# Kernel tuning notes

Hardware: AMD Instinct MI355X
Metric: run time of the kernel (lower is better)

The kernel has to match this reference:

```python
import jax, jax.numpy as jnp
import numpy as np

N, D_IN, D_OUT = 8192, 1024, 1024

def setup_inputs() -> dict:
    key = jax.random.key(0)
    kx, kq, kk, kv = jax.random.split(key, 4)
    # Linear weights stored as [in_dim, out_dim] (torch stores [out,in]; we pre-transpose)
    s = 1.0 / np.sqrt(D_IN)
    return {
        "x": jax.random.normal(kx, (N, D_IN), dtype=jnp.float32),
        "Wq": jax.random.uniform(kq, (D_IN, D_OUT), dtype=jnp.float32, minval=-s, maxval=s),
        "Wk": jax.random.uniform(kk, (D_IN, D_OUT), dtype=jnp.float32, minval=-s, maxval=s),
        "Wv": jax.random.uniform(kv, (D_IN, D_OUT), dtype=jnp.float32, minval=-s, maxval=s),
    }

def reference(x, Wq, Wk, Wv):
    # Faithful to source: query_w = keys_L(x), key_w = queries_L(x) -- a name swap
    # that is just a relabeling of independent random weights. The earlier
    # parameter matmuls in the source are dead code (overwritten) and omitted.
    q = x @ Wk          # [N, D_OUT]
    k = x @ Wq          # [N, D_OUT]
    v = x @ Wv          # [N, D_OUT]
    scores = (q @ k.T) / jnp.sqrt(jnp.asarray(D_OUT, dtype=q.dtype))  # [N, N]
    weights = jax.nn.softmax(scores, axis=-1)
    return weights @ v  # [N, D_OUT]
```

## Files before the change

kernel.cpp:

```cpp
#include <hip/hip_runtime.h>
#include <hip/hip_bf16.h>
#include <stdint.h>

typedef __bf16 v8bf __attribute__((ext_vector_type(8)));
typedef __bf16 v4bf __attribute__((ext_vector_type(4)));
typedef float  v4f  __attribute__((ext_vector_type(4)));

#define AS1 __attribute__((address_space(1)))
#define AS3 __attribute__((address_space(3)))

__device__ __forceinline__ void load16_lds(const void* g, void* l) {
  __builtin_amdgcn_global_load_lds((const AS1 uint32_t*)g, (AS3 uint32_t*)l, 16, 0, 0);
}

__global__ __launch_bounds__(256) void k_cvt_x(const float* __restrict__ x,
                                               __bf16* __restrict__ xb) {
  size_t i = ((size_t)blockIdx.x * 256 + threadIdx.x) * 4;
  float4 f = *(const float4*)(x + i);
  v4bf b; b[0] = (__bf16)f.x; b[1] = (__bf16)f.y; b[2] = (__bf16)f.z; b[3] = (__bf16)f.w;
  *(v4bf*)(xb + i) = b;
}

__global__ __launch_bounds__(256) void k_wtrans(const float* __restrict__ W,
                                                __bf16* __restrict__ Wt) {
  __shared__ float tile[64][65];
  int r0 = blockIdx.x * 64, c0 = blockIdx.y * 64;
  int t = threadIdx.x;
  #pragma unroll
  for (int p = 0; p < 16; p++) {
    int idx = p * 256 + t; int rr = idx >> 6, cc = idx & 63;
    tile[rr][cc] = W[(size_t)(r0 + rr) * 1024 + c0 + cc];
  }
  __syncthreads();
  #pragma unroll
  for (int p = 0; p < 16; p++) {
    int idx = p * 256 + t; int rr = idx >> 6, cc = idx & 63;
    Wt[(size_t)(c0 + rr) * 1024 + r0 + cc] = (__bf16)tile[cc][rr];
  }
}

__global__ __launch_bounds__(256) void k_vtrans(const __bf16* __restrict__ V,
                                                __bf16* __restrict__ Vt) {
  __shared__ __bf16 tile[64][66];
  int r0 = blockIdx.x * 64, c0 = blockIdx.y * 64;
  int t = threadIdx.x;
  #pragma unroll
  for (int p = 0; p < 16; p++) {
    int idx = p * 256 + t; int rr = idx >> 6, cc = idx & 63;
    tile[rr][cc] = V[(size_t)(r0 + rr) * 1024 + c0 + cc];
  }
  __syncthreads();
  #pragma unroll
  for (int p = 0; p < 16; p++) {
    int idx = p * 256 + t; int rr = idx >> 6, cc = idx & 63;
    Vt[(size_t)(c0 + rr) * 8192 + r0 + cc] = tile[cc][rr];
  }
}

__global__ __launch_bounds__(256) void k_zero(float* __restrict__ p) {
  size_t i = ((size_t)blockIdx.x * 256 + threadIdx.x) * 4;
  *(float4*)(p + i) = make_float4(0.f, 0.f, 0.f, 0.f);
}

__global__ __launch_bounds__(256) void k_combine(const float* __restrict__ p0,
                                                 const float* __restrict__ p1,
                                                 const float* __restrict__ rowsum,
                                                 float* __restrict__ out) {
  size_t i = ((size_t)blockIdx.x * 256 + threadIdx.x) * 4;
  float4 a = *(const float4*)(p0 + i);
  float4 b = *(const float4*)(p1 + i);
  float ri = 1.0f / rowsum[i >> 10];
  float4 o;
  o.x = (a.x + b.x) * ri; o.y = (a.y + b.y) * ri;
  o.z = (a.z + b.z) * ri; o.w = (a.w + b.w) * ri;
  *(float4*)(out + i) = o;
}

template <int EPI>
__global__ __launch_bounds__(512, 2) void gemm256(
    const __bf16* __restrict__ A, const __bf16* __restrict__ B,
    void* __restrict__ Cout, int M, int N, int KS, int lda, int ldb,
    __bf16* __restrict__ qp, __bf16* __restrict__ kp, __bf16* __restrict__ vp,
    float* __restrict__ rowsum)
{
  __shared__ __bf16 Asm[2][256 * 64];
  __shared__ __bf16 Bsm[2][256 * 64];

  const int tid  = threadIdx.x;
  const int wave = tid >> 6, lane = tid & 63;
  const int wm = (wave >> 2) * 128;
  const int wn = (wave & 3) * 64;
  const size_t m0 = (size_t)blockIdx.x * 256;
  const size_t n0 = (size_t)blockIdx.y * 256;
  const int NT = KS >> 6;
  const int kz = blockIdx.z * KS;

  const int srow8   = lane >> 3;
  const int sgchunk = (lane & 7) ^ srow8;
  const int fr  = lane & 15;
  const int hi  = lane >> 4;
  const int flo = lane & 7;

  const size_t slda = (size_t)lda, sldb = (size_t)ldb;

  v4f acc[8][4];
  #pragma unroll
  for (int i = 0; i < 8; i++)
    #pragma unroll
    for (int j = 0; j < 4; j++) acc[i][j] = (v4f)0.f;

  auto stageA = [&](int v, int R0) {
    const int kk = kz + (v < NT ? v : NT - 1) * 64;
    const __bf16* s = A + (m0 + R0 + wave * 8 + srow8) * slda + kk + sgchunk * 8;
    __bf16* d = &Asm[v & 1][(R0 + wave * 8) * 64];
    load16_lds(s, d);
    load16_lds(s + 64 * slda, d + 64 * 64);
  };
  auto stageB = [&](int v, int R0) {
    const int kk = kz + (v < NT ? v : NT - 1) * 64;
    const __bf16* s = B + (n0 + R0 + wave * 8 + srow8) * sldb + kk + sgchunk * 8;
    __bf16* d = &Bsm[v & 1][(R0 + wave * 8) * 64];
    load16_lds(s, d);
    load16_lds(s + 64 * sldb, d + 64 * 64);
  };

  stageA(0, 0); stageA(0, 128);
  stageB(0, 0); stageB(0, 128);
  stageB(1, 0); stageB(1, 128);
  asm volatile("s_waitcnt vmcnt(4)" ::: "memory");
  __builtin_amdgcn_s_barrier();

  v8bf aq[4][2], bA[2][2], bB[2][2];

  for (int t = 0; t < NT; t++) {
    const int c = t & 1;
    const __bf16* Ab = Asm[c];
    const __bf16* Bb = Bsm[c];

    #pragma unroll
    for (int i = 0; i < 4; i++)
      #pragma unroll
      for (int h = 0; h < 2; h++)
        aq[i][h] = *(const v8bf*)(Ab + (wm + i * 16 + fr) * 64 + ((((h << 2) | hi) ^ flo) * 8));
    #pragma unroll
    for (int j = 0; j < 2; j++)
      #pragma unroll
      for (int h = 0; h < 2; h++)
        bA[j][h] = *(const v8bf*)(Bb + (wn + j * 16 + fr) * 64 + ((((h << 2) | hi) ^ flo) * 8));
    stageA(t + 1, 0);
    __builtin_amdgcn_s_barrier();
    asm volatile("s_waitcnt lgkmcnt(0)" ::: "memory");
    __builtin_amdgcn_sched_barrier(0);
    __builtin_amdgcn_s_setprio(1);
    #pragma unroll
    for (int h = 0; h < 2; h++)
      #pragma unroll
      for (int i = 0; i < 4; i++)
        #pragma unroll
        for (int j = 0; j < 2; j++)
          acc[i][j] = __builtin_amdgcn_mfma_f32_16x16x32_bf16(aq[i][h], bA[j][h], acc[i][j], 0, 0, 0);
    __builtin_amdgcn_s_setprio(0);
    __builtin_amdgcn_s_barrier();

    #pragma unroll
    for (int j = 0; j < 2; j++)
      #pragma unroll
      for (int h = 0; h < 2; h++)
        bB[j][h] = *(const v8bf*)(Bb + (wn + (j + 2) * 16 + fr) * 64 + ((((h << 2) | hi) ^ flo) * 8));
    stageA(t + 1, 128);
    __builtin_amdgcn_s_barrier();
    asm volatile("s_waitcnt lgkmcnt(0)" ::: "memory");
    __builtin_amdgcn_sched_barrier(0);
    __builtin_amdgcn_s_setprio(1);
    #pragma unroll
    for (int h = 0; h < 2; h++)
      #pragma unroll
      for (int i = 0; i < 4; i++)
        #pragma unroll
        for (int j = 0; j < 2; j++)
          acc[i][j + 2] = __builtin_amdgcn_mfma_f32_16x16x32_bf16(aq[i][h], bB[j][h], acc[i][j + 2], 0, 0, 0);
    __builtin_amdgcn_s_setprio(0);
    __builtin_amdgcn_s_barrier();

    #pragma unroll
    for (int i = 0; i < 4; i++)
      #pragma unroll
      for (int h = 0; h < 2; h++)
        aq[i][h] = *(const v8bf*)(Ab + (wm + (i + 4) * 16 + fr) * 64 + ((((h << 2) | hi) ^ flo) * 8));
    stageB(t + 2, 0);
    __builtin_amdgcn_s_barrier();
    asm volatile("s_waitcnt lgkmcnt(0)" ::: "memory");
    __builtin_amdgcn_sched_barrier(0);
    __builtin_amdgcn_s_setprio(1);
    #pragma unroll
    for (int h = 0; h < 2; h++)
      #pragma unroll
      for (int i = 0; i < 4; i++)
        #pragma unroll
        for (int j = 0; j < 2; j++)
          acc[i + 4][j + 2] = __builtin_amdgcn_mfma_f32_16x16x32_bf16(aq[i][h], bB[j][h], acc[i + 4][j + 2], 0, 0, 0);
    __builtin_amdgcn_s_setprio(0);
    __builtin_amdgcn_s_barrier();

    stageB(t + 2, 128);
    __builtin_amdgcn_s_barrier();
    __builtin_amdgcn_sched_barrier(0);
    __builtin_amdgcn_s_setprio(1);
    #pragma unroll
    for (int h = 0; h < 2; h++)
      #pragma unroll
      for (int i = 0; i < 4; i++)
        #pragma unroll
        for (int j = 0; j < 2; j++)
          acc[i + 4][j] = __builtin_amdgcn_mfma_f32_16x16x32_bf16(aq[i][h], bA[j][h], acc[i + 4][j], 0, 0, 0);
    __builtin_amdgcn_s_setprio(0);
    asm volatile("s_waitcnt vmcnt(4)" ::: "memory");
    __builtin_amdgcn_s_barrier();
  }

  const int er = (lane >> 4) * 4;
  const int ec = lane & 15;

  if (EPI == 3) {
    float rpart[8][4];
    #pragma unroll
    for (int i = 0; i < 8; i++)
      #pragma unroll
      for (int r = 0; r < 4; r++) rpart[i][r] = 0.f;
    #pragma unroll
    for (int i = 0; i < 8; i++)
      #pragma unroll
      for (int j = 0; j < 4; j++) {
        const size_t col = n0 + wn + j * 16 + ec;
        #pragma unroll
        for (int r = 0; r < 4; r++) {
          const size_t rowg = m0 + wm + i * 16 + er + r;
          float e = __expf(acc[i][j][r]);
          ((__bf16*)Cout)[rowg * (size_t)N + col] = (__bf16)e;
          rpart[i][r] += e;
        }
      }
    #pragma unroll
    for (int i = 0; i < 8; i++)
      #pragma unroll
      for (int r = 0; r < 4; r++) {
        float s = rpart[i][r];
        s += __shfl_xor(s, 1); s += __shfl_xor(s, 2);
        s += __shfl_xor(s, 4); s += __shfl_xor(s, 8);
        if (ec == 0) atomicAdd(&rowsum[m0 + wm + i * 16 + er + r], s);
      }
    return;
  }

  #pragma unroll
  for (int i = 0; i < 8; i++)
    #pragma unroll
    for (int j = 0; j < 4; j++) {
      const size_t col = n0 + wn + j * 16 + ec;
      #pragma unroll
      for (int r = 0; r < 4; r++) {
        const size_t rowg = m0 + wm + i * 16 + er + r;
        float val = acc[i][j][r];
        if (EPI == 1) {
          float* po = (float*)Cout + (size_t)blockIdx.z * ((size_t)M * (size_t)N);
          po[rowg * (size_t)N + col] = val;
        } else {
          const int buf = (int)(col >> 10);
          const size_t cc = col & 1023;
          __bf16* dst = (buf == 0) ? qp : ((buf == 1) ? kp : vp);
          if (buf == 0) val *= 0.03125f;
          dst[rowg * 1024 + cc] = (__bf16)val;
        }
      }
    }
}

extern "C" void kernel_launch(void* const* d_in, const int* in_sizes, int n_in,
                              void* d_out, int out_size, void* d_ws, size_t ws_size,
                              hipStream_t stream) {
  const float* x  = (const float*)d_in[0];
  const float* Wq = (const float*)d_in[1];
  const float* Wk = (const float*)d_in[2];
  const float* Wv = (const float*)d_in[3];
  float* out = (float*)d_out;

  const size_t N = 8192, D = 1024;
  char* ws = (char*)d_ws;
  size_t off = 0;
  __bf16* xb = (__bf16*)(ws + off); off += N * D * 2;
  __bf16* wt = (__bf16*)(ws + off); off += 3 * D * D * 2;
  __bf16* q  = (__bf16*)(ws + off); off += N * D * 2;
  __bf16* k  = (__bf16*)(ws + off); off += N * D * 2;
  __bf16* v  = (__bf16*)(ws + off); off += N * D * 2;
  __bf16* vt = (__bf16*)(ws + off); off += N * D * 2;
  __bf16* S  = (__bf16*)(ws + off); off += N * N * 2;
  float* rowsum = (float*)(ws + off); off += N * 4;
  float* pp = (float*)ws;
  if (ws_size < off) return;

  k_cvt_x<<<dim3(8192), dim3(256), 0, stream>>>(x, xb);
  k_wtrans<<<dim3(16, 16), dim3(256), 0, stream>>>(Wk, wt);
  k_wtrans<<<dim3(16, 16), dim3(256), 0, stream>>>(Wq, wt + D * D);
  k_wtrans<<<dim3(16, 16), dim3(256), 0, stream>>>(Wv, wt + 2 * D * D);
  k_zero<<<dim3(8), dim3(256), 0, stream>>>(rowsum);
  gemm256<2><<<dim3(32, 12), dim3(512), 0, stream>>>(xb, wt, nullptr, 8192, 3072, 1024, 1024, 1024, q, k, v, nullptr);
  k_vtrans<<<dim3(128, 16), dim3(256), 0, stream>>>(v, vt);
  gemm256<3><<<dim3(32, 32), dim3(512), 0, stream>>>(q, k, S, 8192, 8192, 1024, 1024, 1024, nullptr, nullptr, nullptr, rowsum);
  gemm256<1><<<dim3(32, 4, 2), dim3(512), 0, stream>>>(S, vt, pp, 8192, 1024, 4096, 8192, 8192, nullptr, nullptr, nullptr, nullptr);
  k_combine<<<dim3(8192), dim3(256), 0, stream>>>(pp, pp + N * D, rowsum, out);
}
```

Before: 468.4 us.

## Software-pipeline LDS fragment loads across K tiles in GEMM main loop

Restructures the GEMM inner loop so LDS fragment reads for the next K-tile (A low half and B first half) are issued during the last MFMA phase of the current tile. The explicit lgkmcnt(0) waits are dropped, and the loop is unrolled by two with ping-pong register sets. The goal is to hide LDS read latency behind MFMA work and remove stalls between phases. In exchange it raises register pressure and tightens the vmcnt and barrier ordering. It also assumes NT is even.

```diff
diff --git a/kernel.cpp b/kernel.cpp
--- a/kernel.cpp
+++ b/kernel.cpp
@@ -123,33 +123,55 @@
     load16_lds(s, d);
     load16_lds(s + 64 * sldb, d + 64 * 64);
   };
+  auto LD = [&](const __bf16* buf, int R, int h) {
+    return *(const v8bf*)(buf + (R + fr) * 64 + ((((h << 2) | hi) ^ flo) * 8));
+  };
+
+  v8bf aLO[4][2], aHI[4][2], bA0[2][2], bA1[2][2], bB[2][2];
 
   stageA(0, 0); stageA(0, 128);
   stageB(0, 0); stageB(0, 128);
   stageB(1, 0); stageB(1, 128);
   asm volatile("s_waitcnt vmcnt(4)" ::: "memory");
   __builtin_amdgcn_s_barrier();
-
-  v8bf aq[4][2], bA[2][2], bB[2][2];
-
-  for (int t = 0; t < NT; t++) {
-    const int c = t & 1;
-    const __bf16* Ab = Asm[c];
-    const __bf16* Bb = Bsm[c];
+  #pragma unroll
+  for (int i = 0; i < 4; i++)
+    #pragma unroll
+    for (int h = 0; h < 2; h++) aLO[i][h] = LD(Asm[0], wm + i * 16, h);
+  #pragma unroll
+  for (int j = 0; j < 2; j++)
+    #pragma unroll
+    for (int h = 0; h < 2; h++) bA0[j][h] = LD(Bsm[0], wn + j * 16, h);
+
+  auto tile = [&](int t, const __bf16* Ab, const __bf16* Bb,
+                  const __bf16* Abn, const __bf16* Bbn,
+                  v8bf (&bAc)[2][2], v8bf (&bAn)[2][2]) {
+    #pragma unroll
+    for (int j = 0; j < 2; j++)
+      #pragma unroll
+      for (int h = 0; h < 2; h++) bB[j][h] = LD(Bb, wn + (j + 2) * 16, h);
+    stageA(t + 1, 0);
+    __builtin_amdgcn_sched_barrier(0);
+    __builtin_amdgcn_s_barrier();
+    __builtin_amdgcn_sched_barrier(0);
+    __builtin_amdgcn_s_setprio(1);
+    #pragma unroll
+    for (int h = 0; h < 2; h++)
+      #pragma unroll
+      for (int i = 0; i < 4; i++)
+        #pragma unroll
+        for (int j = 0; j < 2; j++)
+          acc[i][j] = __builtin_amdgcn_mfma_f32_16x16x32_bf16(aLO[i][h], bAc[j][h], acc[i][j], 0, 0, 0);
+    __builtin_amdgcn_s_setprio(0);
+    __builtin_amdgcn_s_barrier();
 
     #pragma unroll
     for (int i = 0; i < 4; i++)
       #pragma unroll
-      for (int h = 0; h < 2; h++)
-        aq[i][h] = *(const v8bf*)(Ab + (wm + i * 16 + fr) * 64 + ((((h << 2) | hi) ^ flo) * 8));
-    #pragma unroll
-    for (int j = 0; j < 2; j++)
-      #pragma unroll
-      for (int h = 0; h < 2; h++)
-        bA[j][h] = *(const v8bf*)(Bb + (wn + j * 16 + fr) * 64 + ((((h << 2) | hi) ^ flo) * 8));
-    stageA(t + 1, 0);
-    __builtin_amdgcn_s_barrier();
-    asm volatile("s_waitcnt lgkmcnt(0)" ::: "memory");
+      for (int h = 0; h < 2; h++) aHI[i][h] = LD(Ab, wm + (i + 4) * 16, h);
+    stageA(t + 1, 128);
+    __builtin_amdgcn_sched_barrier(0);
+    __builtin_amdgcn_s_barrier();
     __builtin_amdgcn_sched_barrier(0);
     __builtin_amdgcn_s_setprio(1);
     #pragma unroll
@@ -158,18 +180,13 @@
       for (int i = 0; i < 4; i++)
         #pragma unroll
         for (int j = 0; j < 2; j++)
-          acc[i][j] = __builtin_amdgcn_mfma_f32_16x16x32_bf16(aq[i][h], bA[j][h], acc[i][j], 0, 0, 0);
+          acc[i][j + 2] = __builtin_amdgcn_mfma_f32_16x16x32_bf16(aLO[i][h], bB[j][h], acc[i][j + 2], 0, 0, 0);
     __builtin_amdgcn_s_setprio(0);
     __builtin_amdgcn_s_barrier();
 
-    #pragma unroll
-    for (int j = 0; j < 2; j++)
-      #pragma unroll
-      for (int h = 0; h < 2; h++)
-        bB[j][h] = *(const v8bf*)(Bb + (wn + (j + 2) * 16 + fr) * 64 + ((((h << 2) | hi) ^ flo) * 8));
-    stageA(t + 1, 128);
-    __builtin_amdgcn_s_barrier();
-    asm volatile("s_waitcnt lgkmcnt(0)" ::: "memory");
+    stageB(t + 2, 0);
+    __builtin_amdgcn_sched_barrier(0);
+    __builtin_amdgcn_s_barrier();
     __builtin_amdgcn_sched_barrier(0);
     __builtin_amdgcn_s_setprio(1);
     #pragma unroll
@@ -178,18 +195,24 @@
       for (int i = 0; i < 4; i++)
         #pragma unroll
         for (int j = 0; j < 2; j++)
-          acc[i][j + 2] = __builtin_amdgcn_mfma_f32_16x16x32_bf16(aq[i][h], bB[j][h], acc[i][j + 2], 0, 0, 0);
+          acc[i + 4][j + 2] = __builtin_amdgcn_mfma_f32_16x16x32_bf16(aHI[i][h], bB[j][h], acc[i + 4][j + 2], 0, 0, 0);
     __builtin_amdgcn_s_setprio(0);
-    __builtin_amdgcn_s_barrier();
-
-    #pragma unroll
-    for (int i = 0; i < 4; i++)
-      #pragma unroll
-      for (int h = 0; h < 2; h++)
-        aq[i][h] = *(const v8bf*)(Ab + (wm + (i + 4) * 16 + fr) * 64 + ((((h << 2) | hi) ^ flo) * 8));
-    stageB(t + 2, 0);
-    __builtin_amdgcn_s_barrier();
-    asm volatile("s_waitcnt lgkmcnt(0)" ::: "memory");
+    asm volatile("s_waitcnt vmcnt(2)" ::: "memory");
+    __builtin_amdgcn_s_barrier();
+
+    if (t + 1 < NT) {
+      #pragma unroll
+      for (int i = 0; i < 4; i++)
+        #pragma unroll
+        for (int h = 0; h < 2; h++) aLO[i][h] = LD(Abn, wm + i * 16, h);
+      #pragma unroll
+      for (int j = 0; j < 2; j++)
+        #pragma unroll
+        for (int h = 0; h < 2; h++) bAn[j][h] = LD(Bbn, wn + j * 16, h);
+    }
+    stageB(t + 2, 128);
+    __builtin_amdgcn_sched_barrier(0);
+    __builtin_amdgcn_s_barrier();
     __builtin_amdgcn_sched_barrier(0);
     __builtin_amdgcn_s_setprio(1);
     #pragma unroll
@@ -198,24 +221,14 @@
       for (int i = 0; i < 4; i++)
         #pragma unroll
         for (int j = 0; j < 2; j++)
-          acc[i + 4][j + 2] = __builtin_amdgcn_mfma_f32_16x16x32_bf16(aq[i][h], bB[j][h], acc[i + 4][j + 2], 0, 0, 0);
+          acc[i + 4][j] = __builtin_amdgcn_mfma_f32_16x16x32_bf16(aHI[i][h], bAc[j][h], acc[i + 4][j], 0, 0, 0);
     __builtin_amdgcn_s_setprio(0);
     __builtin_amdgcn_s_barrier();
-
-    stageB(t + 2, 128);
-    __builtin_amdgcn_s_barrier();
-    __builtin_amdgcn_sched_barrier(0);
-    __builtin_amdgcn_s_setprio(1);
-    #pragma unroll
-    for (int h = 0; h < 2; h++)
-      #pragma unroll
-      for (int i = 0; i < 4; i++)
-        #pragma unroll
-        for (int j = 0; j < 2; j++)
-          acc[i + 4][j] = __builtin_amdgcn_mfma_f32_16x16x32_bf16(aq[i][h], bA[j][h], acc[i + 4][j], 0, 0, 0);
-    __builtin_amdgcn_s_setprio(0);
-    asm volatile("s_waitcnt vmcnt(4)" ::: "memory");
-    __builtin_amdgcn_s_barrier();
+  };
+
+  for (int t = 0; t < NT; t += 2) {
+    tile(t,     Asm[0], Bsm[0], Asm[1], Bsm[1], bA0, bA1);
+    tile(t + 1, Asm[1], Bsm[1], Asm[0], Bsm[0], bA1, bA0);
   }
 
   const int er = (lane >> 4) * 4;
```

Result: slower. 682.9 us (+45.8%).
